# Kernel optimization log

Hardware: AMD Instinct MI355X
Metric: run time of the kernel (lower is better)

## Reference

```python
import jax, jax.numpy as jnp
import numpy as np

B, N, D = 4, 4096, 128
H = 128  # hidden_size == input_size (required by residual add)

def setup_inputs() -> dict:
    key = jax.random.key(0)
    kx, kw, kb = jax.random.split(key, 3)
    x = jax.random.normal(kx, (B, N, D), dtype=jnp.float32)
    # nn.Linear(input_size, hidden_size): weight [H, D], bias [H]
    lim = 1.0 / np.sqrt(D)
    W = jax.random.uniform(kw, (H, D), dtype=jnp.float32, minval=-lim, maxval=lim)
    b = jax.random.uniform(kb, (H,), dtype=jnp.float32, minval=-lim, maxval=lim)
    return {"x": x, "W": W, "b": b}

def reference(x, W, b):
    # adj[b,i,j] = <x[b,i], x[b,j]>, relu
    adj = jax.nn.relu(jnp.einsum('bid,bjd->bij', x, x))  # [B,N,N]
    # torch sums over dim=1 (rows) -> per-column sums, then divides columns
    col_sum = adj.sum(axis=1)                 # [B,N]
    adj = adj / col_sum[:, None, :]           # broadcast over dim 1
    out = jnp.einsum('bij,bjd->bid', adj, x)  # aggregate
    out = jnp.tanh(jnp.einsum('bnd,hd->bnh', out, W) + b)
    # Dropout(0.5) treated as eval-mode identity
    return out + x  # residual=True
```

## Files before the change

### kernel.cpp

```cpp
#include <hip/hip_runtime.h>
#include <hip/hip_bf16.h>

#define BN 4
#define NN 4096
#define DD 128

typedef __attribute__((ext_vector_type(8))) __bf16 bf16x8;
typedef __attribute__((ext_vector_type(4))) float f32x4;

typedef union {
  bf16x8 v;
  unsigned int u[4];
  uint2 u2[2];
} pk8;

typedef __attribute__((address_space(1))) const unsigned int* gas_p;
typedef __attribute__((address_space(3))) unsigned int* las_p;

__device__ __forceinline__ void gload16(const void* g, void* l) {
  __builtin_amdgcn_global_load_lds((gas_p)g, (las_p)l, 16, 0, 0);
}
__device__ __forceinline__ void wait_vm0() {
  asm volatile("s_waitcnt vmcnt(0)" ::: "memory");
}
__device__ __forceinline__ unsigned int cvtpk(float lo, float hi) {
  unsigned int r;
  asm("v_cvt_pk_bf16_f32 %0, %1, %2" : "=v"(r) : "v"(lo), "v"(hi));
  return r;
}
__device__ __forceinline__ unsigned int pkrelu(float lo, float hi) {
  return cvtpk(fmaxf(lo, 0.f), fmaxf(hi, 0.f));
}

__device__ inline unsigned short f2bf(float f) {
  unsigned int u = __float_as_uint(f);
  unsigned int r = (u + 0x7FFFu + ((u >> 16) & 1u)) >> 16;
  return (unsigned short)r;
}
__device__ inline float bf2f(unsigned short s) {
  return __uint_as_float(((unsigned int)s) << 16);
}

__global__ __launch_bounds__(256) void k_cvt(const float* __restrict__ x,
                                             unsigned short* __restrict__ xb) {
  int i = (blockIdx.x * 256 + threadIdx.x) * 8;
  float4 a = *(const float4*)(x + i);
  float4 c = *(const float4*)(x + i + 4);
  uint4 o;
  o.x = cvtpk(a.x, a.y);
  o.y = cvtpk(a.z, a.w);
  o.z = cvtpk(c.x, c.y);
  o.w = cvtpk(c.z, c.w);
  *(uint4*)(xb + i) = o;
}

__global__ __launch_bounds__(256, 4) void k_colsum(const unsigned short* __restrict__ xb,
                                                   float* __restrict__ colpart) {
  __shared__ unsigned short XiB[2][64 * 128];
  const int b = blockIdx.y, j0 = blockIdx.x * 128, ic = blockIdx.z;
  const int tid = threadIdx.x, lane = tid & 63, wv = tid >> 6;
  const unsigned short* xbb = xb + b * NN * DD;
  const int g = lane >> 4;
  const int ibeg = ic * (NN / 8);
  const int nt = (NN / 8) / 64;

#pragma unroll
  for (int hb = 0; hb < 2; ++hb)
#pragma unroll
    for (int q = 0; q < 4; ++q) {
      int c = wv * 4 + q;
      int lr = c * 4 + g;
      int gsrc = (lane & 15) ^ (lr & 7);
      gload16(&xbb[(j0 + hb * 64 + lr) * 128 + gsrc * 8], &XiB[hb][c * 512]);
    }
  wait_vm0();
  __syncthreads();

  bf16x8 bfr[2][4];
#pragma unroll
  for (int ni = 0; ni < 2; ++ni)
#pragma unroll
    for (int kk = 0; kk < 4; ++kk) {
      int lr = (wv & 1) * 32 + ni * 16 + (lane & 15);
      bfr[ni][kk] = *(const bf16x8*)&XiB[wv >> 1][lr * 128 + (((kk * 4 + g) ^ (lr & 7)) << 3)];
    }
  __syncthreads();

#pragma unroll
  for (int q = 0; q < 4; ++q) {
    int c = wv * 4 + q;
    int lr = c * 4 + g;
    int gsrc = (lane & 15) ^ (lr & 7);
    gload16(&xbb[(ibeg + lr) * 128 + gsrc * 8], &XiB[1][c * 512]);
  }

  int basek[4];
#pragma unroll
  for (int kk = 0; kk < 4; ++kk)
    basek[kk] = (lane & 15) * 128 + (((kk * 4 + g) ^ (lane & 7)) << 3);

  float colacc0 = 0.f, colacc1 = 0.f;
  for (int t = 0; t < nt; ++t) {
    wait_vm0();
    __syncthreads();
    const int cur = (t + 1) & 1, nxt = t & 1;
    if (t + 1 < nt) {
      const int i1 = ibeg + (t + 1) * 64;
#pragma unroll
      for (int q = 0; q < 4; ++q) {
        int c = wv * 4 + q;
        int lr = c * 4 + g;
        int gsrc = (lane & 15) ^ (lr & 7);
        gload16(&xbb[(i1 + lr) * 128 + gsrc * 8], &XiB[nxt][c * 512]);
      }
    }
    f32x4 a0[4], a1[4];
#pragma unroll
    for (int mj = 0; mj < 4; ++mj) { a0[mj] = (f32x4){}; a1[mj] = (f32x4){}; }
    __builtin_amdgcn_s_setprio(1);
#pragma unroll
    for (int kk = 0; kk < 4; ++kk) {
      bf16x8 ar0 = *(const bf16x8*)&XiB[cur][basek[kk]];
      bf16x8 ar1 = *(const bf16x8*)&XiB[cur][basek[kk] + 1 * 2048];
      bf16x8 ar2 = *(const bf16x8*)&XiB[cur][basek[kk] + 2 * 2048];
      bf16x8 ar3 = *(const bf16x8*)&XiB[cur][basek[kk] + 3 * 2048];
      a0[0] = __builtin_amdgcn_mfma_f32_16x16x32_bf16(ar0, bfr[0][kk], a0[0], 0, 0, 0);
      a1[0] = __builtin_amdgcn_mfma_f32_16x16x32_bf16(ar0, bfr[1][kk], a1[0], 0, 0, 0);
      a0[1] = __builtin_amdgcn_mfma_f32_16x16x32_bf16(ar1, bfr[0][kk], a0[1], 0, 0, 0);
      a1[1] = __builtin_amdgcn_mfma_f32_16x16x32_bf16(ar1, bfr[1][kk], a1[1], 0, 0, 0);
      a0[2] = __builtin_amdgcn_mfma_f32_16x16x32_bf16(ar2, bfr[0][kk], a0[2], 0, 0, 0);
      a1[2] = __builtin_amdgcn_mfma_f32_16x16x32_bf16(ar2, bfr[1][kk], a1[2], 0, 0, 0);
      a0[3] = __builtin_amdgcn_mfma_f32_16x16x32_bf16(ar3, bfr[0][kk], a0[3], 0, 0, 0);
      a1[3] = __builtin_amdgcn_mfma_f32_16x16x32_bf16(ar3, bfr[1][kk], a1[3], 0, 0, 0);
    }
    __builtin_amdgcn_s_setprio(0);
    {
      float s0 = 0.f, s1 = 0.f;
#pragma unroll
      for (int mj = 0; mj < 4; ++mj)
#pragma unroll
        for (int r = 0; r < 4; ++r) {
          s0 += fmaxf(a0[mj][r], 0.f);
          s1 += fmaxf(a1[mj][r], 0.f);
        }
      s0 += __shfl_xor(s0, 16); s0 += __shfl_xor(s0, 32);
      s1 += __shfl_xor(s1, 16); s1 += __shfl_xor(s1, 32);
      colacc0 += s0; colacc1 += s1;
    }
  }
  if (lane < 16) {
    colpart[(ic * BN + b) * NN + j0 + wv * 32 + lane] = colacc0;
    colpart[(ic * BN + b) * NN + j0 + wv * 32 + 16 + lane] = colacc1;
  }
}

__global__ __launch_bounds__(256) void k_ytrans(const float* __restrict__ x,
                                                const float* __restrict__ colpart,
                                                unsigned short* __restrict__ yt) {
  __shared__ unsigned short T[64 * 72];
  const int b = blockIdx.z, j0 = blockIdx.y * 64, d0 = blockIdx.x * 64;
  const int tid = threadIdx.x;
  int jr = tid >> 2, q0 = (tid & 3) * 16;
  float cs = 0.f;
#pragma unroll
  for (int ic = 0; ic < 8; ++ic) cs += colpart[(ic * BN + b) * NN + j0 + jr];
  float inv = 1.0f / cs;
  const float* xr = x + (size_t)(b * NN + j0 + jr) * DD + d0 + q0;
#pragma unroll
  for (int q = 0; q < 4; ++q) {
    float4 v = *(const float4*)(xr + q * 4);
    int dc = q0 + q * 4;
    T[jr * 72 + dc + 0] = f2bf(v.x * inv);
    T[jr * 72 + dc + 1] = f2bf(v.y * inv);
    T[jr * 72 + dc + 2] = f2bf(v.z * inv);
    T[jr * 72 + dc + 3] = f2bf(v.w * inv);
  }
  __syncthreads();
  for (int c = tid; c < 512; c += 256) {
    int dr = c >> 3, jg = c & 7;
    alignas(16) unsigned short tmp[8];
#pragma unroll
    for (int u = 0; u < 8; ++u) tmp[u] = T[(jg * 8 + u) * 72 + dr];
    *(uint4*)&yt[(size_t)(b * DD + d0 + dr) * NN + j0 + jg * 8] = *(const uint4*)tmp;
  }
}

__global__ __launch_bounds__(256, 2) void k_pass2(const unsigned short* __restrict__ xb,
                                                  const unsigned short* __restrict__ yt,
                                                  unsigned short* __restrict__ opart,
                                                  int jc) {
  __shared__ unsigned short XjB[2][64 * 128];
  __shared__ unsigned short YsB[2][128 * 64];
  const int b = blockIdx.y, i0 = blockIdx.x * 128, zc = blockIdx.z;
  const int tid = threadIdx.x, lane = tid & 63, wv = tid >> 6;
  const unsigned short* xbb = xb + b * NN * DD;
  const unsigned short* ytb = yt + (size_t)b * DD * NN;
  const int g = lane >> 4;

  const int jspan = NN / jc;
  const int jbeg = zc * jspan;
  const int nt = jspan / 64;

#pragma unroll
  for (int hb = 0; hb < 2; ++hb)
#pragma unroll
    for (int q = 0; q < 4; ++q) {
      int c = wv * 4 + q;
      int lr = c * 4 + g;
      int gsrc = (lane & 15) ^ (lr & 7);
      gload16(&xbb[(i0 + hb * 64 + lr) * 128 + gsrc * 8], &XjB[hb][c * 512]);
    }
#pragma unroll
  for (int q = 0; q < 4; ++q) {
    int c = wv * 4 + q;
    int dr = c * 8 + (lane >> 3);
    int gsrc = (lane & 7) ^ (dr & 7);
    gload16(&ytb[(size_t)dr * NN + jbeg + gsrc * 8], &YsB[1][c * 512]);
  }
  wait_vm0();
  __syncthreads();

  bf16x8 bfr[2][4];
#pragma unroll
  for (int ni = 0; ni < 2; ++ni)
#pragma unroll
    for (int kk = 0; kk < 4; ++kk) {
      int lr = (wv & 1) * 32 + ni * 16 + (lane & 15);
      bfr[ni][kk] = *(const bf16x8*)&XjB[wv >> 1][lr * 128 + (((kk * 4 + g) ^ (lr & 7)) << 3)];
    }
  __syncthreads();

#pragma unroll
  for (int q = 0; q < 4; ++q) {
    int c = wv * 4 + q;
    int lr = c * 4 + g;
    int gsrc = (lane & 15) ^ (lr & 7);
    gload16(&xbb[(jbeg + lr) * 128 + gsrc * 8], &XjB[1][c * 512]);
  }

  int xjb[4];
#pragma unroll
  for (int kk = 0; kk < 4; ++kk)
    xjb[kk] = (lane & 15) * 128 + (((kk * 4 + g) ^ (lane & 7)) << 3);
  int ysb[2][2];
#pragma unroll
  for (int c = 0; c < 2; ++c)
#pragma unroll
    for (int h = 0; h < 2; ++h) {
      int jq = c * 4 + 2 * h + (g >> 1);
      ysb[c][h] = (lane & 15) * 64 + ((jq ^ (lane & 7)) << 3) + (g & 1) * 4;
    }

  f32x4 oacc0[8], oacc1[8];
#pragma unroll
  for (int n = 0; n < 8; ++n) { oacc0[n] = (f32x4){}; oacc1[n] = (f32x4){}; }

  for (int t = 0; t < nt; ++t) {
    wait_vm0();
    __syncthreads();
    const int cur = (t + 1) & 1, nxt = t & 1;
    if (t + 1 < nt) {
      const int j1 = jbeg + (t + 1) * 64;
#pragma unroll
      for (int q = 0; q < 4; ++q) {
        int c = wv * 4 + q;
        int lr = c * 4 + g;
        int gsrc = (lane & 15) ^ (lr & 7);
        gload16(&xbb[(j1 + lr) * 128 + gsrc * 8], &XjB[nxt][c * 512]);
      }
#pragma unroll
      for (int q = 0; q < 4; ++q) {
        int c = wv * 4 + q;
        int dr = c * 8 + (lane >> 3);
        int gsrc = (lane & 7) ^ (dr & 7);
        gload16(&ytb[(size_t)dr * NN + j1 + gsrc * 8], &YsB[nxt][c * 512]);
      }
    }
    const unsigned short* Xj = XjB[cur];
    const unsigned short* Ys = YsB[cur];

    f32x4 s0[4], s1[4];
#pragma unroll
    for (int mj = 0; mj < 4; ++mj) { s0[mj] = (f32x4){}; s1[mj] = (f32x4){}; }
    __builtin_amdgcn_s_setprio(1);
#pragma unroll
    for (int kk = 0; kk < 4; ++kk) {
      bf16x8 ar0 = *(const bf16x8*)&Xj[xjb[kk]];
      bf16x8 ar1 = *(const bf16x8*)&Xj[xjb[kk] + 1 * 2048];
      bf16x8 ar2 = *(const bf16x8*)&Xj[xjb[kk] + 2 * 2048];
      bf16x8 ar3 = *(const bf16x8*)&Xj[xjb[kk] + 3 * 2048];
      s0[0] = __builtin_amdgcn_mfma_f32_16x16x32_bf16(ar0, bfr[0][kk], s0[0], 0, 0, 0);
      s1[0] = __builtin_amdgcn_mfma_f32_16x16x32_bf16(ar0, bfr[1][kk], s1[0], 0, 0, 0);
      s0[1] = __builtin_amdgcn_mfma_f32_16x16x32_bf16(ar1, bfr[0][kk], s0[1], 0, 0, 0);
      s1[1] = __builtin_amdgcn_mfma_f32_16x16x32_bf16(ar1, bfr[1][kk], s1[1], 0, 0, 0);
      s0[2] = __builtin_amdgcn_mfma_f32_16x16x32_bf16(ar2, bfr[0][kk], s0[2], 0, 0, 0);
      s1[2] = __builtin_amdgcn_mfma_f32_16x16x32_bf16(ar2, bfr[1][kk], s1[2], 0, 0, 0);
      s0[3] = __builtin_amdgcn_mfma_f32_16x16x32_bf16(ar3, bfr[0][kk], s0[3], 0, 0, 0);
      s1[3] = __builtin_amdgcn_mfma_f32_16x16x32_bf16(ar3, bfr[1][kk], s1[3], 0, 0, 0);
    }
    __builtin_amdgcn_s_setprio(0);
    pk8 p00, p01, p10, p11;
    p00.u[0] = pkrelu(s0[0][0], s0[0][1]); p00.u[1] = pkrelu(s0[0][2], s0[0][3]);
    p00.u[2] = pkrelu(s0[1][0], s0[1][1]); p00.u[3] = pkrelu(s0[1][2], s0[1][3]);
    p01.u[0] = pkrelu(s1[0][0], s1[0][1]); p01.u[1] = pkrelu(s1[0][2], s1[0][3]);
    p01.u[2] = pkrelu(s1[1][0], s1[1][1]); p01.u[3] = pkrelu(s1[1][2], s1[1][3]);
    p10.u[0] = pkrelu(s0[2][0], s0[2][1]); p10.u[1] = pkrelu(s0[2][2], s0[2][3]);
    p10.u[2] = pkrelu(s0[3][0], s0[3][1]); p10.u[3] = pkrelu(s0[3][2], s0[3][3]);
    p11.u[0] = pkrelu(s1[2][0], s1[2][1]); p11.u[1] = pkrelu(s1[2][2], s1[2][3]);
    p11.u[2] = pkrelu(s1[3][0], s1[3][1]); p11.u[3] = pkrelu(s1[3][2], s1[3][3]);
    __builtin_amdgcn_s_setprio(1);
#pragma unroll
    for (int n = 0; n < 8; ++n) {
      pk8 bb0, bb1;
      bb0.u2[0] = *(const uint2*)&Ys[ysb[0][0] + n * 1024];
      bb0.u2[1] = *(const uint2*)&Ys[ysb[0][1] + n * 1024];
      bb1.u2[0] = *(const uint2*)&Ys[ysb[1][0] + n * 1024];
      bb1.u2[1] = *(const uint2*)&Ys[ysb[1][1] + n * 1024];
      oacc0[n] = __builtin_amdgcn_mfma_f32_16x16x32_bf16(p00.v, bb0.v, oacc0[n], 0, 0, 0);
      oacc1[n] = __builtin_amdgcn_mfma_f32_16x16x32_bf16(p01.v, bb0.v, oacc1[n], 0, 0, 0);
      oacc0[n] = __builtin_amdgcn_mfma_f32_16x16x32_bf16(p10.v, bb1.v, oacc0[n], 0, 0, 0);
      oacc1[n] = __builtin_amdgcn_mfma_f32_16x16x32_bf16(p11.v, bb1.v, oacc1[n], 0, 0, 0);
    }
    __builtin_amdgcn_s_setprio(0);
  }

  __syncthreads();
  unsigned short* sb = &XjB[0][0];
#pragma unroll
  for (int m = 0; m < 2; ++m)
#pragma unroll
    for (int n = 0; n < 8; ++n)
#pragma unroll
      for (int r = 0; r < 4; ++r) {
        int row = wv * 32 + m * 16 + g * 4 + r;
        int col = n * 16 + (lane & 15);
        sb[row * 128 + col] = f2bf(m == 0 ? oacc0[n][r] : oacc1[n][r]);
      }
  __syncthreads();
  for (int c = tid; c < 2048; c += 256) {
    int row = c >> 4, gq = c & 15;
    *(uint4*)&opart[((size_t)zc * (BN * NN) + b * NN + i0 + row) * DD + gq * 8] =
        *(const uint4*)&sb[row * 128 + gq * 8];
  }
}

__global__ __launch_bounds__(256) void k_final(const unsigned short* __restrict__ opart,
                                               int jc,
                                               const float* __restrict__ W,
                                               const float* __restrict__ bias,
                                               const float* __restrict__ x,
                                               float* __restrict__ out) {
  __shared__ unsigned short Wb[128 * 128];
  __shared__ unsigned short PreS[32 * 128];
  const int tid = threadIdx.x, lane = tid & 63, wv = tid >> 6;
  const int g = lane >> 4;
  const int r0 = blockIdx.x * 32;

  {
    int h = tid >> 1, k0h = (tid & 1) * 8;
    const float* wr = W + h * 128 + k0h * 8;
#pragma unroll
    for (int q = 0; q < 8; ++q) {
      float4 v0 = *(const float4*)(wr + q * 8);
      float4 v1 = *(const float4*)(wr + q * 8 + 4);
      uint4 o;
      o.x = cvtpk(v0.x, v0.y); o.y = cvtpk(v0.z, v0.w);
      o.z = cvtpk(v1.x, v1.y); o.w = cvtpk(v1.z, v1.w);
      int gq = k0h + q;
      *(uint4*)&Wb[h * 128 + ((gq ^ (h & 7)) << 3)] = o;
    }
  }
  for (int c = tid; c < 512; c += 256) {
    int row = c >> 4, gq = c & 15;
    float s[8] = {0.f, 0.f, 0.f, 0.f, 0.f, 0.f, 0.f, 0.f};
    for (int ch = 0; ch < jc; ++ch) {
      uint4 pk = *(const uint4*)&opart[((size_t)ch * (BN * NN) + r0 + row) * DD + gq * 8];
      alignas(16) unsigned short us[8];
      *(uint4*)us = pk;
#pragma unroll
      for (int u = 0; u < 8; ++u) s[u] += bf2f(us[u]);
    }
    uint4 o;
    o.x = cvtpk(s[0], s[1]); o.y = cvtpk(s[2], s[3]);
    o.z = cvtpk(s[4], s[5]); o.w = cvtpk(s[6], s[7]);
    *(uint4*)&PreS[row * 128 + ((gq ^ (row & 7)) << 3)] = o;
  }
  __syncthreads();

  bf16x8 af[2][4], bf[2][4];
#pragma unroll
  for (int m = 0; m < 2; ++m)
#pragma unroll
    for (int kk = 0; kk < 4; ++kk) {
      int row = m * 16 + (lane & 15);
      af[m][kk] = *(const bf16x8*)&PreS[row * 128 + (((kk * 4 + g) ^ (row & 7)) << 3)];
    }
#pragma unroll
  for (int n = 0; n < 2; ++n)
#pragma unroll
    for (int kk = 0; kk < 4; ++kk) {
      int h = wv * 32 + n * 16 + (lane & 15);
      bf[n][kk] = *(const bf16x8*)&Wb[h * 128 + (((kk * 4 + g) ^ (h & 7)) << 3)];
    }

  f32x4 acc[2][2] = {};
#pragma unroll
  for (int kk = 0; kk < 4; ++kk) {
    acc[0][0] = __builtin_amdgcn_mfma_f32_16x16x32_bf16(af[0][kk], bf[0][kk], acc[0][0], 0, 0, 0);
    acc[0][1] = __builtin_amdgcn_mfma_f32_16x16x32_bf16(af[0][kk], bf[1][kk], acc[0][1], 0, 0, 0);
    acc[1][0] = __builtin_amdgcn_mfma_f32_16x16x32_bf16(af[1][kk], bf[0][kk], acc[1][0], 0, 0, 0);
    acc[1][1] = __builtin_amdgcn_mfma_f32_16x16x32_bf16(af[1][kk], bf[1][kk], acc[1][1], 0, 0, 0);
  }

  float bh0 = bias[wv * 32 + (lane & 15)];
  float bh1 = bias[wv * 32 + 16 + (lane & 15)];
#pragma unroll
  for (int m = 0; m < 2; ++m)
#pragma unroll
    for (int n = 0; n < 2; ++n)
#pragma unroll
      for (int r = 0; r < 4; ++r) {
        int row = r0 + m * 16 + g * 4 + r;
        int h = wv * 32 + n * 16 + (lane & 15);
        size_t idx = (size_t)row * 128 + h;
        out[idx] = tanhf(acc[m][n][r] + (n == 0 ? bh0 : bh1)) + x[idx];
      }
}

extern "C" void kernel_launch(void* const* d_in, const int* in_sizes, int n_in,
                              void* d_out, int out_size, void* d_ws, size_t ws_size,
                              hipStream_t stream) {
  (void)in_sizes; (void)n_in; (void)out_size;
  const float* x = (const float*)d_in[0];
  const float* W = (const float*)d_in[1];
  const float* bias = (const float*)d_in[2];
  float* out = (float*)d_out;
  char* ws = (char*)d_ws;
  unsigned short* xb = (unsigned short*)ws;
  unsigned short* yt = (unsigned short*)(ws + (4u << 20));
  float* colpart = (float*)(ws + (8u << 20));
  unsigned short* opart = (unsigned short*)(ws + (9u << 20));

  const size_t need4 = (9u << 20) + 4u * (4u << 20);
  const int jc = (ws_size >= need4) ? 4 : 1;

  k_cvt<<<1024, 256, 0, stream>>>(x, xb);
  k_colsum<<<dim3(32, 4, 8), 256, 0, stream>>>(xb, colpart);
  k_ytrans<<<dim3(2, 64, 4), 256, 0, stream>>>(x, colpart, yt);
  k_pass2<<<dim3(32, 4, jc), 256, 0, stream>>>(xb, yt, opart, jc);
  k_final<<<512, 256, 0, stream>>>(opart, jc, W, bias, x, out);
}
```

Baseline: 83.70 us.

## Load MFMA operands directly from global memory instead of staging through LDS

k_colsum no longer stages X tiles in LDS with async global-to-LDS loads and double buffering. Each wave now reads its A and B fragments straight from global memory into registers, and the launch bound drops to 3 blocks. In k_pass2 the Y-transpose tile is also read directly from global memory per wave rather than through a double-buffered LDS tile, while X stays in LDS. This removes LDS traffic, barriers and the shared-memory footprint, but it loses the prefetch overlap, raises register pressure and sends redundant uncoalesced global and L2 reads across waves.

```diff
diff --git a/kernel.cpp b/kernel.cpp
--- a/kernel.cpp
+++ b/kernel.cpp
@@ -54,86 +54,44 @@
   *(uint4*)(xb + i) = o;
 }
 
-__global__ __launch_bounds__(256, 4) void k_colsum(const unsigned short* __restrict__ xb,
+__global__ __launch_bounds__(256, 3) void k_colsum(const unsigned short* __restrict__ xb,
                                                    float* __restrict__ colpart) {
-  __shared__ unsigned short XiB[2][64 * 128];
   const int b = blockIdx.y, j0 = blockIdx.x * 128, ic = blockIdx.z;
   const int tid = threadIdx.x, lane = tid & 63, wv = tid >> 6;
   const unsigned short* xbb = xb + b * NN * DD;
-  const int g = lane >> 4;
+  const int g = lane >> 4, l15 = lane & 15;
   const int ibeg = ic * (NN / 8);
   const int nt = (NN / 8) / 64;
 
-#pragma unroll
-  for (int hb = 0; hb < 2; ++hb)
-#pragma unroll
-    for (int q = 0; q < 4; ++q) {
-      int c = wv * 4 + q;
-      int lr = c * 4 + g;
-      int gsrc = (lane & 15) ^ (lr & 7);
-      gload16(&xbb[(j0 + hb * 64 + lr) * 128 + gsrc * 8], &XiB[hb][c * 512]);
-    }
-  wait_vm0();
-  __syncthreads();
-
   bf16x8 bfr[2][4];
 #pragma unroll
   for (int ni = 0; ni < 2; ++ni)
 #pragma unroll
     for (int kk = 0; kk < 4; ++kk) {
-      int lr = (wv & 1) * 32 + ni * 16 + (lane & 15);
-      bfr[ni][kk] = *(const bf16x8*)&XiB[wv >> 1][lr * 128 + (((kk * 4 + g) ^ (lr & 7)) << 3)];
-    }
-  __syncthreads();
-
-#pragma unroll
-  for (int q = 0; q < 4; ++q) {
-    int c = wv * 4 + q;
-    int lr = c * 4 + g;
-    int gsrc = (lane & 15) ^ (lr & 7);
-    gload16(&xbb[(ibeg + lr) * 128 + gsrc * 8], &XiB[1][c * 512]);
-  }
-
-  int basek[4];
-#pragma unroll
-  for (int kk = 0; kk < 4; ++kk)
-    basek[kk] = (lane & 15) * 128 + (((kk * 4 + g) ^ (lane & 7)) << 3);
+      int jr = j0 + wv * 32 + ni * 16 + l15;
+      bfr[ni][kk] = *(const bf16x8*)&xbb[(size_t)jr * 128 + (kk * 4 + g) * 8];
+    }
 
   float colacc0 = 0.f, colacc1 = 0.f;
   for (int t = 0; t < nt; ++t) {
-    wait_vm0();
-    __syncthreads();
-    const int cur = (t + 1) & 1, nxt = t & 1;
-    if (t + 1 < nt) {
-      const int i1 = ibeg + (t + 1) * 64;
-#pragma unroll
-      for (int q = 0; q < 4; ++q) {
-        int c = wv * 4 + q;
-        int lr = c * 4 + g;
-        int gsrc = (lane & 15) ^ (lr & 7);
-        gload16(&xbb[(i1 + lr) * 128 + gsrc * 8], &XiB[nxt][c * 512]);
-      }
-    }
+    const int it = ibeg + t * 64;
+    bf16x8 ar[4][4];
+#pragma unroll
+    for (int mj = 0; mj < 4; ++mj)
+#pragma unroll
+      for (int kk = 0; kk < 4; ++kk)
+        ar[mj][kk] = *(const bf16x8*)&xbb[(size_t)(it + mj * 16 + l15) * 128 + (kk * 4 + g) * 8];
+
     f32x4 a0[4], a1[4];
 #pragma unroll
     for (int mj = 0; mj < 4; ++mj) { a0[mj] = (f32x4){}; a1[mj] = (f32x4){}; }
-    __builtin_amdgcn_s_setprio(1);
-#pragma unroll
-    for (int kk = 0; kk < 4; ++kk) {
-      bf16x8 ar0 = *(const bf16x8*)&XiB[cur][basek[kk]];
-      bf16x8 ar1 = *(const bf16x8*)&XiB[cur][basek[kk] + 1 * 2048];
-      bf16x8 ar2 = *(const bf16x8*)&XiB[cur][basek[kk] + 2 * 2048];
-      bf16x8 ar3 = *(const bf16x8*)&XiB[cur][basek[kk] + 3 * 2048];
-      a0[0] = __builtin_amdgcn_mfma_f32_16x16x32_bf16(ar0, bfr[0][kk], a0[0], 0, 0, 0);
-      a1[0] = __builtin_amdgcn_mfma_f32_16x16x32_bf16(ar0, bfr[1][kk], a1[0], 0, 0, 0);
-      a0[1] = __builtin_amdgcn_mfma_f32_16x16x32_bf16(ar1, bfr[0][kk], a0[1], 0, 0, 0);
-      a1[1] = __builtin_amdgcn_mfma_f32_16x16x32_bf16(ar1, bfr[1][kk], a1[1], 0, 0, 0);
-      a0[2] = __builtin_amdgcn_mfma_f32_16x16x32_bf16(ar2, bfr[0][kk], a0[2], 0, 0, 0);
-      a1[2] = __builtin_amdgcn_mfma_f32_16x16x32_bf16(ar2, bfr[1][kk], a1[2], 0, 0, 0);
-      a0[3] = __builtin_amdgcn_mfma_f32_16x16x32_bf16(ar3, bfr[0][kk], a0[3], 0, 0, 0);
-      a1[3] = __builtin_amdgcn_mfma_f32_16x16x32_bf16(ar3, bfr[1][kk], a1[3], 0, 0, 0);
-    }
-    __builtin_amdgcn_s_setprio(0);
+#pragma unroll
+    for (int kk = 0; kk < 4; ++kk)
+#pragma unroll
+      for (int mj = 0; mj < 4; ++mj) {
+        a0[mj] = __builtin_amdgcn_mfma_f32_16x16x32_bf16(ar[mj][kk], bfr[0][kk], a0[mj], 0, 0, 0);
+        a1[mj] = __builtin_amdgcn_mfma_f32_16x16x32_bf16(ar[mj][kk], bfr[1][kk], a1[mj], 0, 0, 0);
+      }
     {
       float s0 = 0.f, s1 = 0.f;
 #pragma unroll
@@ -190,12 +148,11 @@
                                                   unsigned short* __restrict__ opart,
                                                   int jc) {
   __shared__ unsigned short XjB[2][64 * 128];
-  __shared__ unsigned short YsB[2][128 * 64];
   const int b = blockIdx.y, i0 = blockIdx.x * 128, zc = blockIdx.z;
   const int tid = threadIdx.x, lane = tid & 63, wv = tid >> 6;
   const unsigned short* xbb = xb + b * NN * DD;
   const unsigned short* ytb = yt + (size_t)b * DD * NN;
-  const int g = lane >> 4;
+  const int g = lane >> 4, l15 = lane & 15;
 
   const int jspan = NN / jc;
   const int jbeg = zc * jspan;
@@ -207,16 +164,9 @@
     for (int q = 0; q < 4; ++q) {
       int c = wv * 4 + q;
       int lr = c * 4 + g;
-      int gsrc = (lane & 15) ^ (lr & 7);
+      int gsrc = l15 ^ (lr & 7);
       gload16(&xbb[(i0 + hb * 64 + lr) * 128 + gsrc * 8], &XjB[hb][c * 512]);
     }
-#pragma unroll
-  for (int q = 0; q < 4; ++q) {
-    int c = wv * 4 + q;
-    int dr = c * 8 + (lane >> 3);
-    int gsrc = (lane & 7) ^ (dr & 7);
-    gload16(&ytb[(size_t)dr * NN + jbeg + gsrc * 8], &YsB[1][c * 512]);
-  }
   wait_vm0();
   __syncthreads();
 
@@ -225,7 +175,7 @@
   for (int ni = 0; ni < 2; ++ni)
 #pragma unroll
     for (int kk = 0; kk < 4; ++kk) {
-      int lr = (wv & 1) * 32 + ni * 16 + (lane & 15);
+      int lr = (wv & 1) * 32 + ni * 16 + l15;
       bfr[ni][kk] = *(const bf16x8*)&XjB[wv >> 1][lr * 128 + (((kk * 4 + g) ^ (lr & 7)) << 3)];
     }
   __syncthreads();
@@ -234,22 +184,14 @@
   for (int q = 0; q < 4; ++q) {
     int c = wv * 4 + q;
     int lr = c * 4 + g;
-    int gsrc = (lane & 15) ^ (lr & 7);
+    int gsrc = l15 ^ (lr & 7);
     gload16(&xbb[(jbeg + lr) * 128 + gsrc * 8], &XjB[1][c * 512]);
   }
 
   int xjb[4];
 #pragma unroll
   for (int kk = 0; kk < 4; ++kk)
-    xjb[kk] = (lane & 15) * 128 + (((kk * 4 + g) ^ (lane & 7)) << 3);
-  int ysb[2][2];
-#pragma unroll
-  for (int c = 0; c < 2; ++c)
-#pragma unroll
-    for (int h = 0; h < 2; ++h) {
-      int jq = c * 4 + 2 * h + (g >> 1);
-      ysb[c][h] = (lane & 15) * 64 + ((jq ^ (lane & 7)) << 3) + (g & 1) * 4;
-    }
+    xjb[kk] = l15 * 128 + (((kk * 4 + g) ^ (lane & 7)) << 3);
 
   f32x4 oacc0[8], oacc1[8];
 #pragma unroll
@@ -259,26 +201,28 @@
     wait_vm0();
     __syncthreads();
     const int cur = (t + 1) & 1, nxt = t & 1;
+    const int jt = jbeg + t * 64;
     if (t + 1 < nt) {
-      const int j1 = jbeg + (t + 1) * 64;
+      const int j1 = jt + 64;
 #pragma unroll
       for (int q = 0; q < 4; ++q) {
         int c = wv * 4 + q;
         int lr = c * 4 + g;
-        int gsrc = (lane & 15) ^ (lr & 7);
+        int gsrc = l15 ^ (lr & 7);
         gload16(&xbb[(j1 + lr) * 128 + gsrc * 8], &XjB[nxt][c * 512]);
       }
-#pragma unroll
-      for (int q = 0; q < 4; ++q) {
-        int c = wv * 4 + q;
-        int dr = c * 8 + (lane >> 3);
-        int gsrc = (lane & 7) ^ (dr & 7);
-        gload16(&ytb[(size_t)dr * NN + j1 + gsrc * 8], &YsB[nxt][c * 512]);
-      }
-    }
+    }
+    pk8 yf[8][2];
+#pragma unroll
+    for (int n = 0; n < 8; ++n)
+#pragma unroll
+      for (int c = 0; c < 2; ++c) {
+        const unsigned short* yp = ytb + (size_t)(n * 16 + l15) * NN + jt + c * 32 + g * 4;
+        yf[n][c].u2[0] = *(const uint2*)yp;
+        yf[n][c].u2[1] = *(const uint2*)(yp + 16);
+      }
+
     const unsigned short* Xj = XjB[cur];
-    const unsigned short* Ys = YsB[cur];
-
     f32x4 s0[4], s1[4];
 #pragma unroll
     for (int mj = 0; mj < 4; ++mj) { s0[mj] = (f32x4){}; s1[mj] = (f32x4){}; }
@@ -311,15 +255,10 @@
     __builtin_amdgcn_s_setprio(1);
 #pragma unroll
     for (int n = 0; n < 8; ++n) {
-      pk8 bb0, bb1;
-      bb0.u2[0] = *(const uint2*)&Ys[ysb[0][0] + n * 1024];
-      bb0.u2[1] = *(const uint2*)&Ys[ysb[0][1] + n * 1024];
-      bb1.u2[0] = *(const uint2*)&Ys[ysb[1][0] + n * 1024];
-      bb1.u2[1] = *(const uint2*)&Ys[ysb[1][1] + n * 1024];
-      oacc0[n] = __builtin_amdgcn_mfma_f32_16x16x32_bf16(p00.v, bb0.v, oacc0[n], 0, 0, 0);
-      oacc1[n] = __builtin_amdgcn_mfma_f32_16x16x32_bf16(p01.v, bb0.v, oacc1[n], 0, 0, 0);
-      oacc0[n] = __builtin_amdgcn_mfma_f32_16x16x32_bf16(p10.v, bb1.v, oacc0[n], 0, 0, 0);
-      oacc1[n] = __builtin_amdgcn_mfma_f32_16x16x32_bf16(p11.v, bb1.v, oacc1[n], 0, 0, 0);
+      oacc0[n] = __builtin_amdgcn_mfma_f32_16x16x32_bf16(p00.v, yf[n][0].v, oacc0[n], 0, 0, 0);
+      oacc1[n] = __builtin_amdgcn_mfma_f32_16x16x32_bf16(p01.v, yf[n][0].v, oacc1[n], 0, 0, 0);
+      oacc0[n] = __builtin_amdgcn_mfma_f32_16x16x32_bf16(p10.v, yf[n][1].v, oacc0[n], 0, 0, 0);
+      oacc1[n] = __builtin_amdgcn_mfma_f32_16x16x32_bf16(p11.v, yf[n][1].v, oacc1[n], 0, 0, 0);
     }
     __builtin_amdgcn_s_setprio(0);
   }
@@ -333,7 +272,7 @@
 #pragma unroll
       for (int r = 0; r < 4; ++r) {
         int row = wv * 32 + m * 16 + g * 4 + r;
-        int col = n * 16 + (lane & 15);
+        int col = n * 16 + l15;
         sb[row * 128 + col] = f2bf(m == 0 ? oacc0[n][r] : oacc1[n][r]);
       }
   __syncthreads();
```

Result: slower. 215.5 us (+157.4%).

## Triple-buffer Y tiles in pass2 and wait on partial vmcnt

Applied to the files above, without the earlier changes.

Pass2 now keeps three Y-tile buffers in LDS and prefetches the Y tile two iterations ahead, while X tiles stay double-buffered. The loop waits with s_waitcnt vmcnt(4) instead of vmcnt(0), so the next tile's loads can stay in flight during compute. This is meant to hide more global-load latency. It raises LDS use by one 16KB buffer, which may cut occupancy below the two blocks per CU requested by the launch bounds.

```diff
diff --git a/kernel.cpp b/kernel.cpp
--- a/kernel.cpp
+++ b/kernel.cpp
@@ -22,6 +22,9 @@
 }
 __device__ __forceinline__ void wait_vm0() {
   asm volatile("s_waitcnt vmcnt(0)" ::: "memory");
+}
+__device__ __forceinline__ void wait_vm4() {
+  asm volatile("s_waitcnt vmcnt(4)" ::: "memory");
 }
 __device__ __forceinline__ unsigned int cvtpk(float lo, float hi) {
   unsigned int r;
@@ -190,12 +193,12 @@
                                                   unsigned short* __restrict__ opart,
                                                   int jc) {
   __shared__ unsigned short XjB[2][64 * 128];
-  __shared__ unsigned short YsB[2][128 * 64];
+  __shared__ unsigned short YsB[3][128 * 64];
   const int b = blockIdx.y, i0 = blockIdx.x * 128, zc = blockIdx.z;
   const int tid = threadIdx.x, lane = tid & 63, wv = tid >> 6;
   const unsigned short* xbb = xb + b * NN * DD;
   const unsigned short* ytb = yt + (size_t)b * DD * NN;
-  const int g = lane >> 4;
+  const int g = lane >> 4, l15 = lane & 15;
 
   const int jspan = NN / jc;
   const int jbeg = zc * jspan;
@@ -207,77 +210,90 @@
     for (int q = 0; q < 4; ++q) {
       int c = wv * 4 + q;
       int lr = c * 4 + g;
-      int gsrc = (lane & 15) ^ (lr & 7);
+      int gsrc = l15 ^ (lr & 7);
       gload16(&xbb[(i0 + hb * 64 + lr) * 128 + gsrc * 8], &XjB[hb][c * 512]);
     }
+  wait_vm0();
+  __syncthreads();
+
+  bf16x8 bfr[2][4];
+#pragma unroll
+  for (int ni = 0; ni < 2; ++ni)
+#pragma unroll
+    for (int kk = 0; kk < 4; ++kk) {
+      int lr = (wv & 1) * 32 + ni * 16 + l15;
+      bfr[ni][kk] = *(const bf16x8*)&XjB[wv >> 1][lr * 128 + (((kk * 4 + g) ^ (lr & 7)) << 3)];
+    }
+  __syncthreads();
+
+#pragma unroll
+  for (int q = 0; q < 4; ++q) {
+    int c = wv * 4 + q;
+    int lr = c * 4 + g;
+    int gsrc = l15 ^ (lr & 7);
+    gload16(&xbb[(jbeg + lr) * 128 + gsrc * 8], &XjB[0][c * 512]);
+  }
 #pragma unroll
   for (int q = 0; q < 4; ++q) {
     int c = wv * 4 + q;
     int dr = c * 8 + (lane >> 3);
     int gsrc = (lane & 7) ^ (dr & 7);
-    gload16(&ytb[(size_t)dr * NN + jbeg + gsrc * 8], &YsB[1][c * 512]);
-  }
-  wait_vm0();
-  __syncthreads();
-
-  bf16x8 bfr[2][4];
-#pragma unroll
-  for (int ni = 0; ni < 2; ++ni)
-#pragma unroll
-    for (int kk = 0; kk < 4; ++kk) {
-      int lr = (wv & 1) * 32 + ni * 16 + (lane & 15);
-      bfr[ni][kk] = *(const bf16x8*)&XjB[wv >> 1][lr * 128 + (((kk * 4 + g) ^ (lr & 7)) << 3)];
-    }
-  __syncthreads();
-
-#pragma unroll
-  for (int q = 0; q < 4; ++q) {
-    int c = wv * 4 + q;
-    int lr = c * 4 + g;
-    int gsrc = (lane & 15) ^ (lr & 7);
-    gload16(&xbb[(jbeg + lr) * 128 + gsrc * 8], &XjB[1][c * 512]);
+    gload16(&ytb[(size_t)dr * NN + jbeg + gsrc * 8], &YsB[0][c * 512]);
+  }
+  if (1 < nt) {
+#pragma unroll
+    for (int q = 0; q < 4; ++q) {
+      int c = wv * 4 + q;
+      int dr = c * 8 + (lane >> 3);
+      int gsrc = (lane & 7) ^ (dr & 7);
+      gload16(&ytb[(size_t)dr * NN + jbeg + 64 + gsrc * 8], &YsB[1][c * 512]);
+    }
   }
 
   int xjb[4];
 #pragma unroll
   for (int kk = 0; kk < 4; ++kk)
-    xjb[kk] = (lane & 15) * 128 + (((kk * 4 + g) ^ (lane & 7)) << 3);
+    xjb[kk] = l15 * 128 + (((kk * 4 + g) ^ (lane & 7)) << 3);
   int ysb[2][2];
 #pragma unroll
   for (int c = 0; c < 2; ++c)
 #pragma unroll
     for (int h = 0; h < 2; ++h) {
       int jq = c * 4 + 2 * h + (g >> 1);
-      ysb[c][h] = (lane & 15) * 64 + ((jq ^ (lane & 7)) << 3) + (g & 1) * 4;
+      ysb[c][h] = l15 * 64 + ((jq ^ (l15 & 7)) << 3) + (g & 1) * 4;
     }
 
   f32x4 oacc0[8], oacc1[8];
 #pragma unroll
   for (int n = 0; n < 8; ++n) { oacc0[n] = (f32x4){}; oacc1[n] = (f32x4){}; }
 
+  int ybuf = 0;
   for (int t = 0; t < nt; ++t) {
-    wait_vm0();
+    if (t + 1 < nt) wait_vm4(); else wait_vm0();
     __syncthreads();
-    const int cur = (t + 1) & 1, nxt = t & 1;
     if (t + 1 < nt) {
       const int j1 = jbeg + (t + 1) * 64;
 #pragma unroll
       for (int q = 0; q < 4; ++q) {
         int c = wv * 4 + q;
         int lr = c * 4 + g;
-        int gsrc = (lane & 15) ^ (lr & 7);
-        gload16(&xbb[(j1 + lr) * 128 + gsrc * 8], &XjB[nxt][c * 512]);
+        int gsrc = l15 ^ (lr & 7);
+        gload16(&xbb[(j1 + lr) * 128 + gsrc * 8], &XjB[(t + 1) & 1][c * 512]);
       }
-#pragma unroll
-      for (int q = 0; q < 4; ++q) {
-        int c = wv * 4 + q;
-        int dr = c * 8 + (lane >> 3);
-        int gsrc = (lane & 7) ^ (dr & 7);
-        gload16(&ytb[(size_t)dr * NN + j1 + gsrc * 8], &YsB[nxt][c * 512]);
+      if (t + 2 < nt) {
+        const int j2 = jbeg + (t + 2) * 64;
+        int nb = ybuf + 2; if (nb >= 3) nb -= 3;
+#pragma unroll
+        for (int q = 0; q < 4; ++q) {
+          int c = wv * 4 + q;
+          int dr = c * 8 + (lane >> 3);
+          int gsrc = (lane & 7) ^ (dr & 7);
+          gload16(&ytb[(size_t)dr * NN + j2 + gsrc * 8], &YsB[nb][c * 512]);
+        }
       }
     }
-    const unsigned short* Xj = XjB[cur];
-    const unsigned short* Ys = YsB[cur];
+    const unsigned short* Xj = XjB[t & 1];
+    const unsigned short* Ys = YsB[ybuf];
 
     f32x4 s0[4], s1[4];
 #pragma unroll
@@ -322,6 +338,7 @@
       oacc1[n] = __builtin_amdgcn_mfma_f32_16x16x32_bf16(p11.v, bb1.v, oacc1[n], 0, 0, 0);
     }
     __builtin_amdgcn_s_setprio(0);
+    ++ybuf; if (ybuf == 3) ybuf = 0;
   }
 
   __syncthreads();
@@ -333,7 +350,7 @@
 #pragma unroll
       for (int r = 0; r < 4; ++r) {
         int row = wv * 32 + m * 16 + g * 4 + r;
-        int col = n * 16 + (lane & 15);
+        int col = n * 16 + l15;
         sb[row * 128 + col] = f2bf(m == 0 ? oacc0[n][r] : oacc1[n][r]);
       }
   __syncthreads();
```

Result: no change. 83.55 us (-0.2%).
